# Optimization experiments

Measured on AMD Instinct MI355X. Metric: run time of the kernel, lower is better.

The kernel has to match this reference:

```python
import jax, jax.numpy as jnp
import numpy as np

N = 80000          # total nodes
F_IN = 16          # num_features
NUM_GRAPHS = 8
P = N // NUM_GRAPHS
EDGES_PER_GRAPH = 80000   # undirected samples per graph (~avg degree 16 after symmetrize)
OUT_DIM = 20000    # num_nodes (output classes)


def _graclus(src, dst, n, rng):
    """Greedy graclus matching (unweighted): visit nodes in random order, match with
    first unmatched neighbor. Cluster id = min(i, match[i]), relabeled consecutively."""
    perm = np.argsort(src, kind='stable')
    s, d = src[perm], dst[perm]
    starts = np.searchsorted(s, np.arange(n))
    ends = np.searchsorted(s, np.arange(n) + 1)
    match = np.full(n, -1, dtype=np.int64)
    for u in rng.permutation(n):
        if match[u] >= 0:
            continue
        match[u] = u
        for v in d[starts[u]:ends[u]]:
            if v != u and match[v] < 0:
                match[u] = v
                match[v] = u
                break
    rep = np.minimum(np.arange(n), match)
    _, cluster = np.unique(rep, return_inverse=True)
    return cluster.astype(np.int64)


def _pool_edges(src, dst, cluster, n1):
    """max_pool edge pooling: map endpoints to clusters, drop self-loops, coalesce."""
    cs, cd = cluster[src], cluster[dst]
    m = cs != cd
    key = np.unique(cs[m].astype(np.int64) * n1 + cd[m])
    return (key // n1).astype(np.int64), (key % n1).astype(np.int64)


def _glorot(k, shape):
    return jax.random.normal(k, shape, jnp.float32) * (2.0 / (shape[0] + shape[1])) ** 0.5


def setup_inputs() -> dict:
    rng = np.random.default_rng(0)
    srcs, dsts = [], []
    for g in range(NUM_GRAPHS):  # edges only within each graph block
        lo = g * P
        u = rng.integers(0, P, EDGES_PER_GRAPH)
        v = rng.integers(0, P, EDGES_PER_GRAPH)
        m = u != v
        u, v = u[m] + lo, v[m] + lo
        key = np.unique(np.minimum(u, v).astype(np.int64) * N + np.maximum(u, v))
        a, b = key // N, key % N
        srcs += [a, b]
        dsts += [b, a]
    src = np.concatenate(srcs).astype(np.int64)
    dst = np.concatenate(dsts).astype(np.int64)
    batch1 = (np.arange(N) // P).astype(np.int64)

    cluster1 = _graclus(src, dst, N, rng)
    n1 = int(cluster1.max()) + 1
    src2, dst2 = _pool_edges(src, dst, cluster1, n1)
    batch2 = np.zeros(n1, np.int64)
    batch2[cluster1] = batch1
    cluster2 = _graclus(src2, dst2, n1, rng)
    n2 = int(cluster2.max()) + 1
    batch3 = np.zeros(n2, np.int64)
    batch3[cluster2] = batch2

    ks = jax.random.split(jax.random.key(0), 12)
    return dict(
        x=jax.random.normal(ks[0], (N, F_IN), jnp.float32),
        W0a=_glorot(ks[1], (F_IN, 32)), W1a=_glorot(ks[2], (F_IN, 32)),
        b1=jnp.zeros((32,), jnp.float32),
        W0b=_glorot(ks[3], (32, 64)), W1b=_glorot(ks[4], (32, 64)),
        b2=jnp.zeros((64,), jnp.float32),
        fcw1=_glorot(ks[5], (64, 128)), fcb1=jnp.zeros((128,), jnp.float32),
        fcw2=_glorot(ks[6], (128, OUT_DIM)), fcb2=jnp.zeros((OUT_DIM,), jnp.float32),
        edge_index1=jnp.asarray(np.stack([src, dst])),
        cluster1=jnp.asarray(cluster1),
        edge_index2=jnp.asarray(np.stack([src2, dst2])),
        cluster2=jnp.asarray(cluster2),
        batch3=jnp.asarray(batch3),
        n1=n1, n2=n2, n_graphs=NUM_GRAPHS,
    )


def _cheb_relu(x, edge_index, W0, W1, b, n):
    """PyG ChebConv K=2, sym norm, lambda_max=2: out = x@W0 + (L~ x)@W1 + b with
    L~ = L - I = -D^{-1/2} A D^{-1/2}; then ReLU."""
    s, d = edge_index[0], edge_index[1]
    deg = jax.ops.segment_sum(jnp.ones(s.shape[0], x.dtype), d, num_segments=n)
    dinv = jnp.where(deg > 0, deg ** -0.5, 0.0)
    w = -(dinv[s] * dinv[d])                       # [E]
    tx1 = jax.ops.segment_sum(w[:, None] * x[s], d, num_segments=n)  # L~ x
    return jax.nn.relu(x @ W0 + tx1 @ W1 + b)


def reference(x, W0a, W1a, b1, W0b, W1b, b2, fcw1, fcb1, fcw2, fcb2,
              edge_index1, cluster1, edge_index2, cluster2, batch3,
              n1, n2, n_graphs):
    h = _cheb_relu(x, edge_index1, W0a, W1a, b1, x.shape[0])     # [N,32]
    hp = jax.ops.segment_max(h, cluster1, num_segments=n1)        # max_pool -> [n1,32]
    h2 = _cheb_relu(hp, edge_index2, W0b, W1b, b2, n1)            # [n1,64]
    h3 = jax.ops.segment_max(h2, cluster2, num_segments=n2)       # max_pool_x -> [n2,64]
    sums = jax.ops.segment_sum(h3, batch3, num_segments=n_graphs)
    cnt = jax.ops.segment_sum(jnp.ones(h3.shape[0], h3.dtype), batch3, num_segments=n_graphs)
    g = sums / cnt[:, None]                                       # global_mean_pool [G,64]
    g = jax.nn.relu(g @ fcw1 + fcb1)                              # dropout is eval-mode identity
    return g @ fcw2 + fcb2                                        # [G, OUT_DIM]
```

## Files before the change

### kernel.cpp

```cpp
#include <hip/hip_runtime.h>

static inline int idiv(int a, int b) { return (a + b - 1) / b; }

__device__ __forceinline__ int swz8(int bid, int nb) {
    int q = nb >> 3, r = nb & 7;
    int x = bid & 7, c = bid >> 3;
    return (x < r ? x * (q + 1) : r * (q + 1) + (x - r) * q) + c;
}

__global__ void k_zero(float4* __restrict__ p, long n4) {
    long t = (long)blockIdx.x * blockDim.x + threadIdx.x;
    long stride = (long)gridDim.x * blockDim.x;
    for (; t < n4; t += stride) p[t] = make_float4(0.f, 0.f, 0.f, 0.f);
}

__global__ void k_prep1m(const int* __restrict__ src, const int* __restrict__ dst,
                         int* __restrict__ ust, int* __restrict__ uen,
                         int* __restrict__ cntS, const int* __restrict__ cl,
                         int* __restrict__ mcnt, int* __restrict__ mem, int E, int N) {
    int t = blockIdx.x * blockDim.x + threadIdx.x;
    int e0 = t << 2;
    if (e0 < N) {
        if (e0 + 3 < N) {
            int4 c4 = *(const int4*)&cl[e0];
            int cc[4] = {c4.x, c4.y, c4.z, c4.w};
#pragma unroll
            for (int i = 0; i < 4; i++) {
                int slot = atomicAdd(&mcnt[cc[i]], 1);
                if (slot < 2) mem[2 * cc[i] + slot] = e0 + i;
            }
        } else {
            for (int i = 0; i < 4 && e0 + i < N; i++) {
                int c = cl[e0 + i];
                int slot = atomicAdd(&mcnt[c], 1);
                if (slot < 2) mem[2 * c + slot] = e0 + i;
            }
        }
    }
    if (e0 >= E) return;
    if (e0 + 3 < E) {
        int4 s4 = *(const int4*)&src[e0];
        int s[4] = {s4.x, s4.y, s4.z, s4.w};
        int d[4] = {dst[e0], dst[e0 + 1], dst[e0 + 2], dst[e0 + 3]};
        bool hasp = e0 > 0;
        int sp = hasp ? src[e0 - 1] : 0, dp = hasp ? dst[e0 - 1] : 0;
        bool hasn = e0 + 4 < E;
        int sn = hasn ? src[e0 + 4] : 0, dn = hasn ? dst[e0 + 4] : 0;
#pragma unroll
        for (int i = 0; i < 4; i++) {
            if (s[i] >= d[i]) continue;
            atomicAdd(&cntS[d[i]], 1);
            bool pvalid = (i > 0) ? true : hasp;
            int psi = (i > 0) ? s[i - 1] : sp, pdi = (i > 0) ? d[i - 1] : dp;
            bool prevup = pvalid && (psi < pdi);
            if (!pvalid || !prevup || psi != s[i]) ust[s[i]] = e0 + i;
            bool nvalid = (i < 3) ? true : hasn;
            int nsi = (i < 3) ? s[i + 1] : sn, ndi = (i < 3) ? d[i + 1] : dn;
            bool nextup = nvalid && (nsi < ndi);
            if (!nvalid || !nextup || nsi != s[i]) uen[s[i]] = e0 + i + 1;
        }
    } else {
        for (int i = 0; i < 4; i++) {
            int e = e0 + i;
            if (e >= E) break;
            int s = src[e], d = dst[e];
            if (s >= d) continue;
            atomicAdd(&cntS[d], 1);
            bool prevup = false; int ps = -1;
            if (e > 0) { ps = src[e - 1]; prevup = (ps < dst[e - 1]); }
            if (e == 0 || !prevup || ps != s) ust[s] = e;
            bool nextup = false; int ns = -1;
            if (e + 1 < E) { ns = src[e + 1]; nextup = (ns < dst[e + 1]); }
            if (e + 1 == E || !nextup || ns != s) uen[s] = e + 1;
        }
    }
}

__global__ void k_bounds2m(const int* __restrict__ src, int* __restrict__ rs,
                           int* __restrict__ re, const int* __restrict__ cl,
                           int* __restrict__ mcnt, int* __restrict__ mem, int E, int n1) {
    int t = blockIdx.x * blockDim.x + threadIdx.x;
    int e0 = t << 2;
    if (e0 < n1) {
        if (e0 + 3 < n1) {
            int4 c4 = *(const int4*)&cl[e0];
            int cc[4] = {c4.x, c4.y, c4.z, c4.w};
#pragma unroll
            for (int i = 0; i < 4; i++) {
                int slot = atomicAdd(&mcnt[cc[i]], 1);
                if (slot < 2) mem[2 * cc[i] + slot] = e0 + i;
            }
        } else {
            for (int i = 0; i < 4 && e0 + i < n1; i++) {
                int c = cl[e0 + i];
                int slot = atomicAdd(&mcnt[c], 1);
                if (slot < 2) mem[2 * c + slot] = e0 + i;
            }
        }
    }
    if (e0 >= E) return;
    if (e0 + 3 < E) {
        int4 s4 = *(const int4*)&src[e0];
        int s[4] = {s4.x, s4.y, s4.z, s4.w};
        int sp = (e0 > 0) ? src[e0 - 1] : -1;
        int sn = (e0 + 4 < E) ? src[e0 + 4] : -1;
        bool hasn = e0 + 4 < E;
#pragma unroll
        for (int i = 0; i < 4; i++) {
            int prev = (i > 0) ? s[i - 1] : sp;
            if (e0 + i == 0 || prev != s[i]) rs[s[i]] = e0 + i;
            bool nvalid = (i < 3) ? true : hasn;
            int nxt = (i < 3) ? s[i + 1] : sn;
            if (!nvalid || nxt != s[i]) re[s[i]] = e0 + i + 1;
        }
    } else {
        for (int i = 0; i < 4; i++) {
            int e = e0 + i;
            if (e >= E) break;
            int s = src[e];
            if (e == 0 || src[e - 1] != s) rs[s] = e;
            if (e + 1 == E || src[e + 1] != s) re[s] = e + 1;
        }
    }
}

__global__ void k_dinv2(const int* __restrict__ rs, const int* __restrict__ re,
                        float* __restrict__ dinv, int n) {
    int t = blockIdx.x * blockDim.x + threadIdx.x;
    if (t < n) {
        int deg = re[t] - rs[t];
        dinv[t] = (deg > 0) ? rsqrtf((float)deg) : 0.0f;
    }
}

__global__ void k_scan_blk(const int* __restrict__ cnt, int* __restrict__ offs,
                           int* __restrict__ blksum, int n) {
    __shared__ int ts[256];
    int blk = blockIdx.x;
    int tid = threadIdx.x;
    int i0 = blk * 1024 + tid * 4;
    int a0 = 0, a1 = 0, a2 = 0, a3 = 0;
    if (i0 + 3 < n) {
        int4 v = *(const int4*)&cnt[i0];
        a0 = v.x; a1 = v.y; a2 = v.z; a3 = v.w;
    } else {
        if (i0 + 0 < n) a0 = cnt[i0 + 0];
        if (i0 + 1 < n) a1 = cnt[i0 + 1];
        if (i0 + 2 < n) a2 = cnt[i0 + 2];
    }
    int tsum = a0 + a1 + a2 + a3;
    ts[tid] = tsum;
    __syncthreads();
    for (int off = 1; off < 256; off <<= 1) {
        int v = (tid >= off) ? ts[tid - off] : 0;
        __syncthreads();
        ts[tid] += v;
        __syncthreads();
    }
    int ex = ts[tid] - tsum;
    if (tid == 255) blksum[blk] = ts[255];
    int p0 = ex, p1 = ex + a0, p2 = p1 + a1, p3 = p2 + a2;
    if (i0 + 3 < n) {
        *(int4*)&offs[i0] = make_int4(p0, p1, p2, p3);
    } else {
        if (i0 + 0 < n) offs[i0 + 0] = p0;
        if (i0 + 1 < n) offs[i0 + 1] = p1;
        if (i0 + 2 < n) offs[i0 + 2] = p2;
    }
}

__global__ void k_scan_tot(int* __restrict__ blksum, int nblk) {
    __shared__ int s[1024];
    int tid = threadIdx.x;
    int v = (tid < nblk) ? blksum[tid] : 0;
    s[tid] = v;
    __syncthreads();
    for (int off = 1; off < 1024; off <<= 1) {
        int t = (tid >= off) ? s[tid - off] : 0;
        __syncthreads();
        s[tid] += t;
        __syncthreads();
    }
    if (tid < nblk) blksum[tid] = s[tid] - v;
}

__global__ void k_scan_add_dinv(int* __restrict__ offs, int* __restrict__ cursor,
                                const int* __restrict__ blksum, const int* __restrict__ cntS,
                                const int* __restrict__ ust, const int* __restrict__ uen,
                                float* __restrict__ dinv, int n) {
    int t = blockIdx.x * blockDim.x + threadIdx.x;
    if (t < n) {
        int v = offs[t] + blksum[t >> 10];
        offs[t] = v;
        cursor[t] = v;
        int deg = cntS[t] + uen[t] - ust[t];
        dinv[t] = (deg > 0) ? rsqrtf((float)deg) : 0.0f;
    }
}

__global__ void k_fillS(const int* __restrict__ src, const int* __restrict__ dst,
                        int* __restrict__ cursor, int* __restrict__ csr, int E) {
    int t = blockIdx.x * blockDim.x + threadIdx.x;
    int e0 = t << 2;
    if (e0 >= E) return;
    if (e0 + 3 < E) {
        int4 s4 = *(const int4*)&src[e0];
        int s[4] = {s4.x, s4.y, s4.z, s4.w};
        int d[4] = {dst[e0], dst[e0 + 1], dst[e0 + 2], dst[e0 + 3]};
#pragma unroll
        for (int i = 0; i < 4; i++) {
            if (s[i] < d[i]) {
                int pos = atomicAdd(&cursor[d[i]], 1);
                csr[pos] = s[i];
            }
        }
    } else {
        for (int i = 0; i < 4; i++) {
            int e = e0 + i;
            if (e >= E) break;
            int s = src[e], d = dst[e];
            if (s < d) {
                int pos = atomicAdd(&cursor[d], 1);
                csr[pos] = s;
            }
        }
    }
}

__global__ void k_gather1v(const int* __restrict__ ust, const int* __restrict__ uen,
                           const int* __restrict__ dst1, const int* __restrict__ offsS,
                           const int* __restrict__ cntS, const int* __restrict__ csrS,
                           const float* __restrict__ dinv, const float* __restrict__ xin,
                           float* __restrict__ tx, int n) {
    int vb = swz8(blockIdx.x, gridDim.x);
    int t = vb * blockDim.x + threadIdx.x;
    int d = t >> 2, ln = t & 3, fo = ln << 2;
    if (d >= n) return;
    float ax = 0.f, ay = 0.f, az = 0.f, aw = 0.f;
    int e0 = ust[d], e1 = uen[d];
    for (int j = e0; j < e1; j += 4) {
        int myj = j + ln;
        int s = 0; float w = 0.f;
        if (myj < e1) { s = dst1[myj]; w = dinv[s]; }
#pragma unroll
        for (int k = 0; k < 4; k++) {
            if (j + k >= e1) break;
            int sk = __shfl(s, k, 4);
            float wk = __shfl(w, k, 4);
            float4 v = *(const float4*)&xin[((long)sk << 4) + fo];
            ax += wk * v.x; ay += wk * v.y; az += wk * v.z; aw += wk * v.w;
        }
    }
    int i0 = offsS[d], i1 = i0 + cntS[d];
    for (int j = i0; j < i1; j += 4) {
        int myj = j + ln;
        int s = 0; float w = 0.f;
        if (myj < i1) { s = csrS[myj]; w = dinv[s]; }
#pragma unroll
        for (int k = 0; k < 4; k++) {
            if (j + k >= i1) break;
            int sk = __shfl(s, k, 4);
            float wk = __shfl(w, k, 4);
            float4 v = *(const float4*)&xin[((long)sk << 4) + fo];
            ax += wk * v.x; ay += wk * v.y; az += wk * v.z; aw += wk * v.w;
        }
    }
    float wd = -dinv[d];
    *(float4*)&tx[((long)d << 4) + fo] = make_float4(wd * ax, wd * ay, wd * az, wd * aw);
}

__global__ void k_gather2v(const int* __restrict__ rs, const int* __restrict__ re,
                           const int* __restrict__ dst2, const float* __restrict__ dinv,
                           const float* __restrict__ xin, float* __restrict__ tx, int n) {
    int vb = swz8(blockIdx.x, gridDim.x);
    int t = vb * blockDim.x + threadIdx.x;
    int d = t >> 3, ln = t & 7, fo = ln << 2;
    if (d >= n) return;
    float ax = 0.f, ay = 0.f, az = 0.f, aw = 0.f;
    int j0 = rs[d], j1 = re[d];
    for (int j = j0; j < j1; j += 8) {
        int myj = j + ln;
        int s = 0; float w = 0.f;
        if (myj < j1) { s = dst2[myj]; w = dinv[s]; }
#pragma unroll
        for (int k = 0; k < 8; k++) {
            if (j + k >= j1) break;
            int sk = __shfl(s, k, 8);
            float wk = __shfl(w, k, 8);
            float4 v = *(const float4*)&xin[((long)sk << 5) + fo];
            ax += wk * v.x; ay += wk * v.y; az += wk * v.z; aw += wk * v.w;
        }
    }
    float wd = -dinv[d];
    *(float4*)&tx[((long)d << 5) + fo] = make_float4(wd * ax, wd * ay, wd * az, wd * aw);
}

__global__ void k_cheb1(const float* __restrict__ x, const float* __restrict__ tx,
                        const float* __restrict__ W0, const float* __restrict__ W1,
                        const float* __restrict__ b, float* __restrict__ h, int N) {
    int t = blockIdx.x * blockDim.x + threadIdx.x;
    int n = t >> 3, jj = (t & 7) << 2;
    if (n >= N) return;
    const float4* xr = (const float4*)(x + (long)n * 16);
    const float4* tr = (const float4*)(tx + (long)n * 16);
    float4 bv = *(const float4*)(b + jj);
    float a0 = bv.x, a1 = bv.y, a2 = bv.z, a3 = bv.w;
#pragma unroll
    for (int k4 = 0; k4 < 4; k4++) {
        float4 xv = xr[k4];
        float4 tv = tr[k4];
        float xs[4] = {xv.x, xv.y, xv.z, xv.w};
        float ts[4] = {tv.x, tv.y, tv.z, tv.w};
#pragma unroll
        for (int c = 0; c < 4; c++) {
            int k = k4 * 4 + c;
            float4 w0 = *(const float4*)(W0 + k * 32 + jj);
            float4 w1 = *(const float4*)(W1 + k * 32 + jj);
            a0 += xs[c] * w0.x + ts[c] * w1.x;
            a1 += xs[c] * w0.y + ts[c] * w1.y;
            a2 += xs[c] * w0.z + ts[c] * w1.z;
            a3 += xs[c] * w0.w + ts[c] * w1.w;
        }
    }
    *(float4*)(h + ((long)n << 5) + jj) =
        make_float4(fmaxf(a0, 0.f), fmaxf(a1, 0.f), fmaxf(a2, 0.f), fmaxf(a3, 0.f));
}

__global__ void k_pool1(const int* __restrict__ mcnt, const int* __restrict__ mem,
                        const float* __restrict__ h, float* __restrict__ hp, int n1) {
    int t = blockIdx.x * blockDim.x + threadIdx.x;
    int c = t >> 3, fo = (t & 7) << 2;
    if (c >= n1) return;
    int m0 = mem[2 * c];
    float4 v = *(const float4*)&h[((long)m0 << 5) + fo];
    if (mcnt[c] > 1) {
        int m1 = mem[2 * c + 1];
        float4 u = *(const float4*)&h[((long)m1 << 5) + fo];
        v.x = fmaxf(v.x, u.x); v.y = fmaxf(v.y, u.y);
        v.z = fmaxf(v.z, u.z); v.w = fmaxf(v.w, u.w);
    }
    *(float4*)&hp[((long)c << 5) + fo] = v;
}

__global__ void k_cheb2(const float* __restrict__ xp, const float* __restrict__ tx,
                        const float* __restrict__ W0, const float* __restrict__ W1,
                        const float* __restrict__ b, float* __restrict__ h2, int n1) {
    int t = blockIdx.x * blockDim.x + threadIdx.x;
    int n = t >> 4, jj = (t & 15) << 2;
    if (n >= n1) return;
    const float4* xr = (const float4*)(xp + (long)n * 32);
    const float4* tr = (const float4*)(tx + (long)n * 32);
    float4 bv = *(const float4*)(b + jj);
    float a0 = bv.x, a1 = bv.y, a2 = bv.z, a3 = bv.w;
#pragma unroll
    for (int k4 = 0; k4 < 8; k4++) {
        float4 xv = xr[k4];
        float4 tv = tr[k4];
        float xs[4] = {xv.x, xv.y, xv.z, xv.w};
        float ts[4] = {tv.x, tv.y, tv.z, tv.w};
#pragma unroll
        for (int c = 0; c < 4; c++) {
            int k = k4 * 4 + c;
            float4 w0 = *(const float4*)(W0 + k * 64 + jj);
            float4 w1 = *(const float4*)(W1 + k * 64 + jj);
            a0 += xs[c] * w0.x + ts[c] * w1.x;
            a1 += xs[c] * w0.y + ts[c] * w1.y;
            a2 += xs[c] * w0.z + ts[c] * w1.z;
            a3 += xs[c] * w0.w + ts[c] * w1.w;
        }
    }
    *(float4*)(h2 + ((long)n << 6) + jj) =
        make_float4(fmaxf(a0, 0.f), fmaxf(a1, 0.f), fmaxf(a2, 0.f), fmaxf(a3, 0.f));
}

__global__ void k_gsum2(const float* __restrict__ h2, const int* __restrict__ mcnt,
                        const int* __restrict__ mem, const int* __restrict__ batch,
                        float* __restrict__ gsum, float* __restrict__ gcnt, int n2) {
    __shared__ float s[8 * 64];
    __shared__ float sc[8];
    for (int i = threadIdx.x; i < 512; i += blockDim.x) s[i] = 0.0f;
    if (threadIdx.x < 8) sc[threadIdx.x] = 0.0f;
    __syncthreads();
    long total = (long)n2 * 16;
    long stride = (long)gridDim.x * blockDim.x;
    for (long t = (long)blockIdx.x * blockDim.x + threadIdx.x; t < total; t += stride) {
        int c = (int)(t >> 4), fo = (int)(t & 15) << 2;
        int m0 = mem[2 * c];
        float4 v = *(const float4*)&h2[((long)m0 << 6) + fo];
        if (mcnt[c] > 1) {
            int m1 = mem[2 * c + 1];
            float4 u = *(const float4*)&h2[((long)m1 << 6) + fo];
            v.x = fmaxf(v.x, u.x); v.y = fmaxf(v.y, u.y);
            v.z = fmaxf(v.z, u.z); v.w = fmaxf(v.w, u.w);
        }
        int g = batch[c];
        atomicAdd(&s[g * 64 + fo + 0], v.x);
        atomicAdd(&s[g * 64 + fo + 1], v.y);
        atomicAdd(&s[g * 64 + fo + 2], v.z);
        atomicAdd(&s[g * 64 + fo + 3], v.w);
        if (fo == 0) atomicAdd(&sc[g], 1.0f);
    }
    __syncthreads();
    for (int i = threadIdx.x; i < 512; i += blockDim.x) atomicAdd(&gsum[i], s[i]);
    if (threadIdx.x < 8) atomicAdd(&gcnt[threadIdx.x], sc[threadIdx.x]);
}

__global__ void k_fc12(const float* __restrict__ gsum, const float* __restrict__ gcnt,
                       const float* __restrict__ fcw1, const float* __restrict__ fcb1,
                       const float* __restrict__ fcw2, const float* __restrict__ fcb2,
                       float* __restrict__ out, int OUT) {
    __shared__ float sm[8 * 64];
    __shared__ float sg[8 * 128];
    int tid = threadIdx.x;
    for (int i = tid; i < 512; i += blockDim.x) {
        float c = gcnt[i >> 6];
        sm[i] = (c > 0.0f) ? gsum[i] / c : 0.0f;
    }
    __syncthreads();
    for (int e = tid; e < 1024; e += blockDim.x) {
        int gi = e >> 7, j = e & 127;
        float acc = fcb1[j];
#pragma unroll 8
        for (int k = 0; k < 64; k++) acc += sm[gi * 64 + k] * fcw1[k * 128 + j];
        sg[e] = fmaxf(acc, 0.0f);
    }
    __syncthreads();
    int o = blockIdx.x * blockDim.x + tid;
    if (o >= OUT) return;
    float bias = fcb2[o];
    float acc[8];
#pragma unroll
    for (int gi = 0; gi < 8; gi++) acc[gi] = bias;
    for (int k = 0; k < 128; k++) {
        float w = fcw2[(long)k * OUT + o];
#pragma unroll
        for (int gi = 0; gi < 8; gi++) acc[gi] += sg[gi * 128 + k] * w;
    }
#pragma unroll
    for (int gi = 0; gi < 8; gi++) out[(long)gi * OUT + o] = acc[gi];
}

extern "C" void kernel_launch(void* const* d_in, const int* in_sizes, int n_in,
                              void* d_out, int out_size, void* d_ws, size_t ws_size,
                              hipStream_t stream) {
    const float* x    = (const float*)d_in[0];
    const float* W0a  = (const float*)d_in[1];
    const float* W1a  = (const float*)d_in[2];
    const float* b1   = (const float*)d_in[3];
    const float* W0b  = (const float*)d_in[4];
    const float* W1b  = (const float*)d_in[5];
    const float* b2   = (const float*)d_in[6];
    const float* fcw1 = (const float*)d_in[7];
    const float* fcb1 = (const float*)d_in[8];
    const float* fcw2 = (const float*)d_in[9];
    const float* fcb2 = (const float*)d_in[10];
    const int* ei1    = (const int*)d_in[11];
    const int* cl1    = (const int*)d_in[12];
    const int* ei2    = (const int*)d_in[13];
    const int* cl2    = (const int*)d_in[14];
    const int* b3     = (const int*)d_in[15];

    const int N  = in_sizes[12];
    const int E1 = in_sizes[11] / 2;
    const int E2 = in_sizes[13] / 2;
    const int n1 = in_sizes[14];
    const int n2 = in_sizes[15];
    const int G  = 8;
    const int OUT = out_size / G;

    const int nmax = (N > n1) ? N : n1;

    auto rnd = [](size_t b) { return (b + 255) & ~(size_t)255; };
    size_t cntB  = rnd((size_t)N * 4);
    size_t ustB  = rnd((size_t)N * 4);
    size_t uenB  = rnd((size_t)N * 4);
    size_t rs2B  = rnd((size_t)n1 * 4);
    size_t re2B  = rnd((size_t)n1 * 4);
    size_t mc1B  = rnd((size_t)n1 * 4);
    size_t mc2B  = rnd((size_t)n2 * 4);
    size_t smlB  = rnd((512 + 8) * 4);
    size_t offB  = rnd((size_t)N * 4);
    size_t curB  = rnd((size_t)N * 4);
    size_t csrB  = rnd((size_t)(E1 / 2 + 64) * 4);
    size_t dinvB = rnd((size_t)nmax * 4);
    size_t blkB  = rnd((size_t)1024 * 4);
    size_t mem1B = rnd((size_t)n1 * 2 * 4);
    size_t mem2B = rnd((size_t)n2 * 2 * 4);
    size_t hpB   = rnd((size_t)n1 * 32 * 4);
    size_t txB   = rnd((size_t)(((long)N * 16 > (long)n1 * 32) ? (long)N * 16 : (long)n1 * 32) * 4);

    char* base = (char*)d_ws;
    char* p = base;
    int*   cntS   = (int*)p;           p += cntB;
    int*   ust    = (int*)p;           p += ustB;
    int*   uen    = (int*)p;           p += uenB;
    int*   rs2    = (int*)p;           p += rs2B;
    int*   re2    = (int*)p;           p += re2B;
    int*   mcnt1  = (int*)p;           p += mc1B;
    int*   mcnt2  = (int*)p;           p += mc2B;
    float* gsum   = (float*)p;         p += smlB;
    float* gcnt   = gsum + 512;
    size_t zeroB  = (size_t)(p - base);
    int*   offsS  = (int*)p;           p += offB;
    int*   cursorS= (int*)p;           p += curB;
    int*   csrS   = (int*)p;           p += csrB;
    float* dinv   = (float*)p;         p += dinvB;
    int*   blksum = (int*)p;           p += blkB;
    int*   mem1   = (int*)p;           p += mem1B;
    int*   mem2   = (int*)p;           p += mem2B;
    float* hp     = (float*)p;         p += hpB;
    float* txA    = (float*)p;         p += txB;
    float* hbuf   = (float*)p;
    (void)ws_size;

    dim3 B(256);
    {
        long n4 = (long)(zeroB / 16);
        int g = idiv((int)((n4 < 1048576) ? n4 : 1048576), 256);
        if (g < 1) g = 1;
        if (g > 4096) g = 4096;
        k_zero<<<g, B, 0, stream>>>((float4*)base, n4);
    }

    {
        int nblk = idiv(N, 1024);
        int maxEN = (E1 > N) ? E1 : N;
        k_prep1m<<<idiv(maxEN, 1024), B, 0, stream>>>(ei1, ei1 + E1, ust, uen, cntS,
                                                      cl1, mcnt1, mem1, E1, N);
        k_scan_blk<<<nblk, B, 0, stream>>>(cntS, offsS, blksum, N);
        k_scan_tot<<<1, 1024, 0, stream>>>(blksum, nblk);
        k_scan_add_dinv<<<idiv(N, 256), B, 0, stream>>>(offsS, cursorS, blksum, cntS, ust, uen,
                                                        dinv, N);
        k_fillS<<<idiv(E1, 1024), B, 0, stream>>>(ei1, ei1 + E1, cursorS, csrS, E1);
        k_gather1v<<<idiv(N * 4, 256), B, 0, stream>>>(ust, uen, ei1 + E1, offsS, cntS, csrS,
                                                       dinv, x, txA, N);
        k_cheb1<<<idiv(N * 8, 256), B, 0, stream>>>(x, txA, W0a, W1a, b1, hbuf, N);
        k_pool1<<<idiv(n1 * 8, 256), B, 0, stream>>>(mcnt1, mem1, hbuf, hp, n1);
    }

    {
        int maxEn = (E2 > n1) ? E2 : n1;
        k_bounds2m<<<idiv(maxEn, 1024), B, 0, stream>>>(ei2, rs2, re2, cl2, mcnt2, mem2, E2, n1);
        k_dinv2<<<idiv(n1, 256), B, 0, stream>>>(rs2, re2, dinv, n1);
        k_gather2v<<<idiv(n1 * 8, 256), B, 0, stream>>>(rs2, re2, ei2 + E2, dinv, hp, txA, n1);
        k_cheb2<<<idiv(n1 * 16, 256), B, 0, stream>>>(hp, txA, W0b, W1b, b2, hbuf, n1);
    }

    int gb = idiv(n2 * 16, 256);
    if (gb > 256) gb = 256;
    k_gsum2<<<gb, B, 0, stream>>>(hbuf, mcnt2, mem2, b3, gsum, gcnt, n2);
    k_fc12<<<idiv(OUT, 256), B, 0, stream>>>(gsum, gcnt, fcw1, fcb1, fcw2, fcb2,
                                             (float*)d_out, OUT);
}
```

Measured before the change: 214.2 us.

## Prescale features by dinv, fold scan total and pooling into neighboring kernels

Each node's features are now pre-multiplied by its inverse sqrt degree (y = dinv*x) inside existing per-node kernels. The gather kernels can then sum neighbor rows directly instead of gathering a dinv value per edge and shuffling it. The separate block-sum scan kernel is folded into the scan-add kernel, with every block rescanning the small block-sum array in shared memory. Layer-1 max pooling is merged into the layer-2 bounds/membership kernel. Together this removes two launches and per-edge weight loads, at the cost of writing extra scaled-feature buffers that reuse the h buffer.

```diff
diff --git a/kernel.cpp b/kernel.cpp
--- a/kernel.cpp
+++ b/kernel.cpp
@@ -76,28 +76,31 @@
     }
 }
 
-__global__ void k_bounds2m(const int* __restrict__ src, int* __restrict__ rs,
-                           int* __restrict__ re, const int* __restrict__ cl,
-                           int* __restrict__ mcnt, int* __restrict__ mem, int E, int n1) {
+__global__ void k_bounds2mp(const int* __restrict__ src, int* __restrict__ rs,
+                            int* __restrict__ re, const int* __restrict__ cl,
+                            int* __restrict__ mcnt2, int* __restrict__ mem2,
+                            const int* __restrict__ mcnt1, const int* __restrict__ mem1,
+                            const float* __restrict__ h, float* __restrict__ hp,
+                            int E, int n1) {
     int t = blockIdx.x * blockDim.x + threadIdx.x;
+    if (t < n1 * 8) {
+        int c = t >> 3, fo = (t & 7) << 2;
+        int m0 = mem1[2 * c];
+        float4 v = *(const float4*)&h[((long)m0 << 5) + fo];
+        if (mcnt1[c] > 1) {
+            int m1 = mem1[2 * c + 1];
+            float4 u = *(const float4*)&h[((long)m1 << 5) + fo];
+            v.x = fmaxf(v.x, u.x); v.y = fmaxf(v.y, u.y);
+            v.z = fmaxf(v.z, u.z); v.w = fmaxf(v.w, u.w);
+        }
+        *(float4*)&hp[((long)c << 5) + fo] = v;
+    }
+    if (t < n1) {
+        int c = cl[t];
+        int slot = atomicAdd(&mcnt2[c], 1);
+        if (slot < 2) mem2[2 * c + slot] = t;
+    }
     int e0 = t << 2;
-    if (e0 < n1) {
-        if (e0 + 3 < n1) {
-            int4 c4 = *(const int4*)&cl[e0];
-            int cc[4] = {c4.x, c4.y, c4.z, c4.w};
-#pragma unroll
-            for (int i = 0; i < 4; i++) {
-                int slot = atomicAdd(&mcnt[cc[i]], 1);
-                if (slot < 2) mem[2 * cc[i] + slot] = e0 + i;
-            }
-        } else {
-            for (int i = 0; i < 4 && e0 + i < n1; i++) {
-                int c = cl[e0 + i];
-                int slot = atomicAdd(&mcnt[c], 1);
-                if (slot < 2) mem[2 * c + slot] = e0 + i;
-            }
-        }
-    }
     if (e0 >= E) return;
     if (e0 + 3 < E) {
         int4 s4 = *(const int4*)&src[e0];
@@ -124,12 +127,20 @@
     }
 }
 
-__global__ void k_dinv2(const int* __restrict__ rs, const int* __restrict__ re,
-                        float* __restrict__ dinv, int n) {
+__global__ void k_dinv2y(const int* __restrict__ rs, const int* __restrict__ re,
+                         float* __restrict__ dinv, const float* __restrict__ hp,
+                         float* __restrict__ y2, int n) {
     int t = blockIdx.x * blockDim.x + threadIdx.x;
-    if (t < n) {
-        int deg = re[t] - rs[t];
-        dinv[t] = (deg > 0) ? rsqrtf((float)deg) : 0.0f;
+    if (t >= n) return;
+    int deg = re[t] - rs[t];
+    float w = (deg > 0) ? rsqrtf((float)deg) : 0.0f;
+    dinv[t] = w;
+    const float4* hr = (const float4*)(hp + (long)t * 32);
+    float4* yr = (float4*)(y2 + (long)t * 32);
+#pragma unroll
+    for (int i = 0; i < 8; i++) {
+        float4 v = hr[i];
+        yr[i] = make_float4(w * v.x, w * v.y, w * v.z, w * v.w);
     }
 }
 
@@ -169,32 +180,42 @@
     }
 }
 
-__global__ void k_scan_tot(int* __restrict__ blksum, int nblk) {
-    __shared__ int s[1024];
+__global__ void k_scan_add_dinv_y(int* __restrict__ offs, int* __restrict__ cursor,
+                                  const int* __restrict__ blksum, const int* __restrict__ cntS,
+                                  const int* __restrict__ ust, const int* __restrict__ uen,
+                                  float* __restrict__ dinv, const float* __restrict__ xin,
+                                  float* __restrict__ y1, int n, int nblk) {
+    __shared__ int s[128];
+    __shared__ int orig[128];
     int tid = threadIdx.x;
-    int v = (tid < nblk) ? blksum[tid] : 0;
-    s[tid] = v;
+    if (tid < 128) {
+        int v = (tid < nblk) ? blksum[tid] : 0;
+        s[tid] = v; orig[tid] = v;
+    }
     __syncthreads();
-    for (int off = 1; off < 1024; off <<= 1) {
-        int t = (tid >= off) ? s[tid - off] : 0;
+    for (int off = 1; off < 128; off <<= 1) {
+        int v = 0;
+        if (tid < 128 && tid >= off) v = s[tid - off];
         __syncthreads();
-        s[tid] += t;
+        if (tid < 128) s[tid] += v;
         __syncthreads();
     }
-    if (tid < nblk) blksum[tid] = s[tid] - v;
-}
-
-__global__ void k_scan_add_dinv(int* __restrict__ offs, int* __restrict__ cursor,
-                                const int* __restrict__ blksum, const int* __restrict__ cntS,
-                                const int* __restrict__ ust, const int* __restrict__ uen,
-                                float* __restrict__ dinv, int n) {
-    int t = blockIdx.x * blockDim.x + threadIdx.x;
-    if (t < n) {
-        int v = offs[t] + blksum[t >> 10];
-        offs[t] = v;
-        cursor[t] = v;
-        int deg = cntS[t] + uen[t] - ust[t];
-        dinv[t] = (deg > 0) ? rsqrtf((float)deg) : 0.0f;
+    int t = blockIdx.x * blockDim.x + tid;
+    if (t >= n) return;
+    int blk = t >> 10;
+    int base = s[blk] - orig[blk];
+    int v = offs[t] + base;
+    offs[t] = v;
+    cursor[t] = v;
+    int deg = cntS[t] + uen[t] - ust[t];
+    float w = (deg > 0) ? rsqrtf((float)deg) : 0.0f;
+    dinv[t] = w;
+    const float4* xr = (const float4*)(xin + (long)t * 16);
+    float4* yr = (float4*)(y1 + (long)t * 16);
+#pragma unroll
+    for (int i = 0; i < 4; i++) {
+        float4 u = xr[i];
+        yr[i] = make_float4(w * u.x, w * u.y, w * u.z, w * u.w);
     }
 }
 
@@ -227,10 +248,10 @@
     }
 }
 
-__global__ void k_gather1v(const int* __restrict__ ust, const int* __restrict__ uen,
+__global__ void k_gather1y(const int* __restrict__ ust, const int* __restrict__ uen,
                            const int* __restrict__ dst1, const int* __restrict__ offsS,
                            const int* __restrict__ cntS, const int* __restrict__ csrS,
-                           const float* __restrict__ dinv, const float* __restrict__ xin,
+                           const float* __restrict__ dinv, const float* __restrict__ y1,
                            float* __restrict__ tx, int n) {
     int vb = swz8(blockIdx.x, gridDim.x);
     int t = vb * blockDim.x + threadIdx.x;
@@ -240,38 +261,34 @@
     int e0 = ust[d], e1 = uen[d];
     for (int j = e0; j < e1; j += 4) {
         int myj = j + ln;
-        int s = 0; float w = 0.f;
-        if (myj < e1) { s = dst1[myj]; w = dinv[s]; }
+        int s = (myj < e1) ? dst1[myj] : 0;
 #pragma unroll
         for (int k = 0; k < 4; k++) {
             if (j + k >= e1) break;
             int sk = __shfl(s, k, 4);
-            float wk = __shfl(w, k, 4);
-            float4 v = *(const float4*)&xin[((long)sk << 4) + fo];
-            ax += wk * v.x; ay += wk * v.y; az += wk * v.z; aw += wk * v.w;
+            float4 v = *(const float4*)&y1[((long)sk << 4) + fo];
+            ax += v.x; ay += v.y; az += v.z; aw += v.w;
         }
     }
     int i0 = offsS[d], i1 = i0 + cntS[d];
     for (int j = i0; j < i1; j += 4) {
         int myj = j + ln;
-        int s = 0; float w = 0.f;
-        if (myj < i1) { s = csrS[myj]; w = dinv[s]; }
+        int s = (myj < i1) ? csrS[myj] : 0;
 #pragma unroll
         for (int k = 0; k < 4; k++) {
             if (j + k >= i1) break;
             int sk = __shfl(s, k, 4);
-            float wk = __shfl(w, k, 4);
-            float4 v = *(const float4*)&xin[((long)sk << 4) + fo];
-            ax += wk * v.x; ay += wk * v.y; az += wk * v.z; aw += wk * v.w;
+            float4 v = *(const float4*)&y1[((long)sk << 4) + fo];
+            ax += v.x; ay += v.y; az += v.z; aw += v.w;
         }
     }
     float wd = -dinv[d];
     *(float4*)&tx[((long)d << 4) + fo] = make_float4(wd * ax, wd * ay, wd * az, wd * aw);
 }
 
-__global__ void k_gather2v(const int* __restrict__ rs, const int* __restrict__ re,
+__global__ void k_gather2y(const int* __restrict__ rs, const int* __restrict__ re,
                            const int* __restrict__ dst2, const float* __restrict__ dinv,
-                           const float* __restrict__ xin, float* __restrict__ tx, int n) {
+                           const float* __restrict__ y2, float* __restrict__ tx, int n) {
     int vb = swz8(blockIdx.x, gridDim.x);
     int t = vb * blockDim.x + threadIdx.x;
     int d = t >> 3, ln = t & 7, fo = ln << 2;
@@ -280,15 +297,13 @@
     int j0 = rs[d], j1 = re[d];
     for (int j = j0; j < j1; j += 8) {
         int myj = j + ln;
-        int s = 0; float w = 0.f;
-        if (myj < j1) { s = dst2[myj]; w = dinv[s]; }
+        int s = (myj < j1) ? dst2[myj] : 0;
 #pragma unroll
         for (int k = 0; k < 8; k++) {
             if (j + k >= j1) break;
             int sk = __shfl(s, k, 8);
-            float wk = __shfl(w, k, 8);
-            float4 v = *(const float4*)&xin[((long)sk << 5) + fo];
-            ax += wk * v.x; ay += wk * v.y; az += wk * v.z; aw += wk * v.w;
+            float4 v = *(const float4*)&y2[((long)sk << 5) + fo];
+            ax += v.x; ay += v.y; az += v.z; aw += v.w;
         }
     }
     float wd = -dinv[d];
@@ -324,22 +339,6 @@
     }
     *(float4*)(h + ((long)n << 5) + jj) =
         make_float4(fmaxf(a0, 0.f), fmaxf(a1, 0.f), fmaxf(a2, 0.f), fmaxf(a3, 0.f));
-}
-
-__global__ void k_pool1(const int* __restrict__ mcnt, const int* __restrict__ mem,
-                        const float* __restrict__ h, float* __restrict__ hp, int n1) {
-    int t = blockIdx.x * blockDim.x + threadIdx.x;
-    int c = t >> 3, fo = (t & 7) << 2;
-    if (c >= n1) return;
-    int m0 = mem[2 * c];
-    float4 v = *(const float4*)&h[((long)m0 << 5) + fo];
-    if (mcnt[c] > 1) {
-        int m1 = mem[2 * c + 1];
-        float4 u = *(const float4*)&h[((long)m1 << 5) + fo];
-        v.x = fmaxf(v.x, u.x); v.y = fmaxf(v.y, u.y);
-        v.z = fmaxf(v.z, u.z); v.w = fmaxf(v.w, u.w);
-    }
-    *(float4*)&hp[((long)c << 5) + fo] = v;
 }
 
 __global__ void k_cheb2(const float* __restrict__ xp, const float* __restrict__ tx,
@@ -513,6 +512,11 @@
     float* hbuf   = (float*)p;
     (void)ws_size;
 
+    float* y1 = hbuf;
+    float* h1 = hbuf;
+    float* y2 = hbuf;
+    float* h2 = hbuf;
+
     dim3 B(256);
     {
         long n4 = (long)(zeroB / 16);
@@ -528,27 +532,27 @@
         k_prep1m<<<idiv(maxEN, 1024), B, 0, stream>>>(ei1, ei1 + E1, ust, uen, cntS,
                                                       cl1, mcnt1, mem1, E1, N);
         k_scan_blk<<<nblk, B, 0, stream>>>(cntS, offsS, blksum, N);
-        k_scan_tot<<<1, 1024, 0, stream>>>(blksum, nblk);
-        k_scan_add_dinv<<<idiv(N, 256), B, 0, stream>>>(offsS, cursorS, blksum, cntS, ust, uen,
-                                                        dinv, N);
+        k_scan_add_dinv_y<<<idiv(N, 256), B, 0, stream>>>(offsS, cursorS, blksum, cntS, ust, uen,
+                                                          dinv, x, y1, N, nblk);
         k_fillS<<<idiv(E1, 1024), B, 0, stream>>>(ei1, ei1 + E1, cursorS, csrS, E1);
-        k_gather1v<<<idiv(N * 4, 256), B, 0, stream>>>(ust, uen, ei1 + E1, offsS, cntS, csrS,
-                                                       dinv, x, txA, N);
-        k_cheb1<<<idiv(N * 8, 256), B, 0, stream>>>(x, txA, W0a, W1a, b1, hbuf, N);
-        k_pool1<<<idiv(n1 * 8, 256), B, 0, stream>>>(mcnt1, mem1, hbuf, hp, n1);
+        k_gather1y<<<idiv(N * 4, 256), B, 0, stream>>>(ust, uen, ei1 + E1, offsS, cntS, csrS,
+                                                       dinv, y1, txA, N);
+        k_cheb1<<<idiv(N * 8, 256), B, 0, stream>>>(x, txA, W0a, W1a, b1, h1, N);
     }
 
     {
-        int maxEn = (E2 > n1) ? E2 : n1;
-        k_bounds2m<<<idiv(maxEn, 1024), B, 0, stream>>>(ei2, rs2, re2, cl2, mcnt2, mem2, E2, n1);
-        k_dinv2<<<idiv(n1, 256), B, 0, stream>>>(rs2, re2, dinv, n1);
-        k_gather2v<<<idiv(n1 * 8, 256), B, 0, stream>>>(rs2, re2, ei2 + E2, dinv, hp, txA, n1);
-        k_cheb2<<<idiv(n1 * 16, 256), B, 0, stream>>>(hp, txA, W0b, W1b, b2, hbuf, n1);
+        int e4 = idiv(E2, 4);
+        int maxT = (e4 > n1 * 8) ? e4 : n1 * 8;
+        k_bounds2mp<<<idiv(maxT, 256), B, 0, stream>>>(ei2, rs2, re2, cl2, mcnt2, mem2,
+                                                       mcnt1, mem1, h1, hp, E2, n1);
+        k_dinv2y<<<idiv(n1, 256), B, 0, stream>>>(rs2, re2, dinv, hp, y2, n1);
+        k_gather2y<<<idiv(n1 * 8, 256), B, 0, stream>>>(rs2, re2, ei2 + E2, dinv, y2, txA, n1);
+        k_cheb2<<<idiv(n1 * 16, 256), B, 0, stream>>>(hp, txA, W0b, W1b, b2, h2, n1);
     }
 
     int gb = idiv(n2 * 16, 256);
     if (gb > 256) gb = 256;
-    k_gsum2<<<gb, B, 0, stream>>>(hbuf, mcnt2, mem2, b3, gsum, gcnt, n2);
+    k_gsum2<<<gb, B, 0, stream>>>(h2, mcnt2, mem2, b3, gsum, gcnt, n2);
     k_fc12<<<idiv(OUT, 256), B, 0, stream>>>(gsum, gcnt, fcw1, fcb1, fcw2, fcb2,
                                              (float*)d_out, OUT);
 }
```

After: 212.9 us, median of 2. No clear change (-0.6%).
